# Kernel optimization log

Hardware: AMD Instinct MI355X
Metric: run time of the kernel (lower is better)

## Reference

```python
import jax, jax.numpy as jnp
import numpy as np

B, H, W, C = 4, 64, 64, 256       # C == number_of_filters // 2
NOF = 512
CA = NOF // 8                      # f/g projection dim = 64
CH = NOF // 2                      # h / output projection dim = 256 (== C)


def setup_inputs() -> dict:
    key = jax.random.key(0)
    ks = jax.random.split(key, 10)
    sc = 1.0 / np.sqrt(C)
    x = jax.random.normal(ks[0], (B, H, W, C), jnp.float32)
    Wf = jax.random.normal(ks[1], (C, CA), jnp.float32) * sc
    bf = jnp.zeros((CA,), jnp.float32)
    Wg = jax.random.normal(ks[2], (C, CA), jnp.float32) * sc
    bg = jnp.zeros((CA,), jnp.float32)
    Wh = jax.random.normal(ks[3], (C, CH), jnp.float32) * sc
    bh = jnp.zeros((CH,), jnp.float32)
    Wo = jax.random.normal(ks[4], (CH, CH), jnp.float32) * (1.0 / np.sqrt(CH))
    bo = jnp.zeros((CH,), jnp.float32)
    gamma = jax.random.normal(ks[5], (1,), jnp.float32) * 0.1
    return {"x": x, "Wf": Wf, "bf": bf, "Wg": Wg, "bg": bg,
            "Wh": Wh, "bh": bh, "Wo": Wo, "bo": bo, "gamma": gamma}


def reference(x, Wf, bf, Wg, bg, Wh, bh, Wo, bo, gamma):
    b, h, w, c = x.shape
    n = h * w
    # 1x1 conv projections == per-pixel matmuls over channels
    f = (jnp.einsum('bhwc,cd->bhwd', x, Wf) + bf).reshape(b, n, -1)   # [B,N,CA]
    g = (jnp.einsum('bhwc,cd->bhwd', x, Wg) + bg).reshape(b, n, -1)   # [B,N,CA]
    hh = (jnp.einsum('bhwc,cd->bhwd', x, Wh) + bh).reshape(b, n, -1)  # [B,N,CH]
    # s = g @ f^T : full spatial attention scores [B,N,N]
    s = jnp.einsum('bnd,bmd->bnm', g, f)
    beta = jax.nn.softmax(s, axis=-1)
    o = jnp.einsum('bnm,bmc->bnc', beta, hh).reshape(b, h, w, c)      # CH == C
    # post-attention 1x1 conv
    o2 = jnp.einsum('bhwc,cd->bhwd', o, Wo) + bo
    y = gamma * o2 + x
    return y
```

## Files before the change

kernel.cpp:

```cpp
#include <hip/hip_runtime.h>

typedef __bf16  bf16x8 __attribute__((ext_vector_type(8)));
typedef short   s16x8  __attribute__((ext_vector_type(8)));
typedef float   f32x4  __attribute__((ext_vector_type(4)));
typedef float   f32x16 __attribute__((ext_vector_type(16)));
typedef int     i32x2  __attribute__((ext_vector_type(2)));

#define LOG2E 1.44269504088896f
#define SM_M2 (44.0f * LOG2E)

__device__ __forceinline__ unsigned short f2bf(float f){
  unsigned u = __builtin_bit_cast(unsigned, f);
  return (unsigned short)((u + 0x7fffu + ((u >> 16) & 1u)) >> 16);
}

__device__ __forceinline__ int cvtpk_bf16(float a, float b){
  int r; asm("v_cvt_pk_bf16_f32 %0, %1, %2" : "=v"(r) : "v"(a), "v"(b)); return r;
}

__device__ __forceinline__ float bfhalf2f(unsigned short u){
  unsigned v = ((unsigned)u) << 16; return __builtin_bit_cast(float, v);
}

#define OFF_WTFG 0u
#define OFF_WHT  65536u
#define OFF_WOT  196608u
#define OFF_XBF  327680u
#define OFF_F    8716288u
#define OFF_G    10813440u
#define OFF_HT   12910592u
#define OFF_PART 21299200u
#define OFF_LP   38076416u

__global__ __launch_bounds__(256) void prep(const float* __restrict__ x,
                                            const float* __restrict__ Wf, const float* __restrict__ Wg,
                                            const float* __restrict__ Wh, const float* __restrict__ Wo,
                                            unsigned short* __restrict__ xbf,
                                            unsigned short* __restrict__ WTfg,
                                            unsigned short* __restrict__ WhT,
                                            unsigned short* __restrict__ WoT){
  int bid = blockIdx.x;
  if (bid < 2048) {
    int t = bid * 256 + threadIdx.x;
    const f32x4* xp = (const f32x4*)x;
    f32x4 a = xp[2 * t], b = xp[2 * t + 1];
    s16x8 o;
    o[0] = (short)f2bf(a[0]); o[1] = (short)f2bf(a[1]); o[2] = (short)f2bf(a[2]); o[3] = (short)f2bf(a[3]);
    o[4] = (short)f2bf(b[0]); o[5] = (short)f2bf(b[1]); o[6] = (short)f2bf(b[2]); o[7] = (short)f2bf(b[3]);
    ((s16x8*)xbf)[t] = o;
  } else {
    int t = (bid - 2048) * 256 + threadIdx.x;
    if (t < 32768) {
      int n = t >> 8, k = t & 255;
      float v = (n < 64) ? Wf[k * 64 + n] : Wg[k * 64 + (n - 64)];
      WTfg[t] = f2bf(v);
    } else if (t < 98304) {
      int i = t - 32768; int n = i >> 8, k = i & 255;
      WhT[i] = f2bf(Wh[k * 256 + n]);
    } else {
      int i = t - 98304; int n = i >> 8, k = i & 255;
      WoT[i] = f2bf(Wo[k * 256 + n]);
    }
  }
}

__global__ __launch_bounds__(256) void proj(const unsigned short* __restrict__ xbf,
                                            const unsigned short* __restrict__ WTfg,
                                            const unsigned short* __restrict__ WhT,
                                            const float* __restrict__ bfv, const float* __restrict__ bgv,
                                            const float* __restrict__ bhv,
                                            unsigned short* __restrict__ fK, unsigned short* __restrict__ gQ,
                                            unsigned short* __restrict__ hT){
  int lane = threadIdx.x & 63, widx = threadIdx.x >> 6;
  int l15 = lane & 15, g4 = lane >> 4;
  int bid = blockIdx.x;
  if (bid < 1024) {
    int w = bid * 4 + widx;
    int c0 = (w & 15) * 16;
    int pb = (w >> 4) * 64;
    bf16x8 a[8];
    const unsigned short* wr = WhT + (c0 + l15) * 256 + g4 * 8;
#pragma unroll
    for (int kb = 0; kb < 8; kb++) a[kb] = *(const bf16x8*)(wr + kb * 32);
#pragma unroll
    for (int pt = 0; pt < 4; pt++) {
      int p0 = pb + pt * 16;
      f32x4 acc = {0.f, 0.f, 0.f, 0.f};
      const unsigned short* xr = xbf + (p0 + l15) * 256 + g4 * 8;
#pragma unroll
      for (int kb = 0; kb < 8; kb++) {
        bf16x8 b = *(const bf16x8*)(xr + kb * 32);
        acc = __builtin_amdgcn_mfma_f32_16x16x32_bf16(a[kb], b, acc, 0, 0, 0);
      }
      int bq = p0 >> 12, n0 = p0 & 4095;
      unsigned short* op = hT + bq * (256 * 4096) + n0 + l15;
#pragma unroll
      for (int r = 0; r < 4; r++) {
        int c = c0 + g4 * 4 + r;
        op[c * 4096] = f2bf(acc[r] + bhv[c]);
      }
    }
  } else {
    int w = (bid - 1024) * 4 + widx;
    int p0 = w * 16;
    bf16x8 a[8];
    const unsigned short* xr = xbf + (p0 + l15) * 256 + g4 * 8;
#pragma unroll
    for (int kb = 0; kb < 8; kb++) a[kb] = *(const bf16x8*)(xr + kb * 32);
#pragma unroll
    for (int ct = 0; ct < 8; ct++) {
      int c0 = ct * 16;
      f32x4 acc = {0.f, 0.f, 0.f, 0.f};
      const unsigned short* wr = WTfg + (c0 + l15) * 256 + g4 * 8;
#pragma unroll
      for (int kb = 0; kb < 8; kb++) {
        bf16x8 b = *(const bf16x8*)(wr + kb * 32);
        acc = __builtin_amdgcn_mfma_f32_16x16x32_bf16(a[kb], b, acc, 0, 0, 0);
      }
      float bias = (ct < 4) ? bfv[c0 + l15] : bgv[c0 - 64 + l15];
      unsigned short* outp = (ct < 4) ? (fK + c0 + l15) : (gQ + (c0 - 64) + l15);
#pragma unroll
      for (int r = 0; r < 4; r++) {
        int row = p0 + g4 * 4 + r;
        outp[row * 64] = f2bf(acc[r] + bias);
      }
    }
  }
}

__global__ __launch_bounds__(512, 2) void attn1(const unsigned short* __restrict__ fK,
                                                const unsigned short* __restrict__ gQ,
                                                const unsigned short* __restrict__ hT,
                                                unsigned short* __restrict__ part,
                                                float* __restrict__ lpart){
  __shared__ __attribute__((aligned(16))) char smem[81920];
  const int tid  = threadIdx.x;
  const int lane = tid & 63, w = tid >> 6;
  const int l31  = lane & 31, hi = lane >> 5;
  const int qh   = w >> 1, cs = w & 1;
  const int b    = blockIdx.x & 3;
  const int rest = blockIdx.x >> 2;
  const int qb   = rest >> 1;
  const int kh   = rest & 1;
  const int q0   = qb * 128 + qh * 32;
  const int kbase = kh * 2048;

  const unsigned short* fKb = fK + (size_t)b * 4096 * 64;
  const unsigned short* gQb = gQ + (size_t)b * 4096 * 64;
  const unsigned short* hTb = hT + (size_t)b * 256 * 4096;

  bf16x8 qfr[4];
#pragma unroll
  for (int c4 = 0; c4 < 4; c4++)
    qfr[c4] = *(const bf16x8*)(gQb + (size_t)(q0 + l31) * 64 + c4 * 16 + hi * 8);

  char* buf0 = smem;
  char* buf1 = smem + 32768;
  char* kb0  = smem + 65536;
  char* kb1  = smem + 73728;

  auto STAGE = [&](char* vbuf, char* kbuf, int m0){
    int r = lane >> 3, gl = lane & 7;
#pragma unroll
    for (int k = 0; k < 4; k++){
      int c = 32 * w + k * 8 + r;
      const unsigned short* gp = hTb + (size_t)c * 4096 + m0 + ((gl ^ (c & 7)) * 8);
      __builtin_amdgcn_global_load_lds((const __attribute__((address_space(1))) unsigned int*)gp,
          (__attribute__((address_space(3))) unsigned int*)(vbuf + ((4 * w + k) << 10)), 16, 0, 0);
    }
    {
      int row = 8 * w + r;
      const unsigned short* gp = fKb + (size_t)(m0 + row) * 64 + ((gl ^ r) * 8);
      __builtin_amdgcn_global_load_lds((const __attribute__((address_space(1))) unsigned int*)gp,
          (__attribute__((address_space(3))) unsigned int*)(kbuf + (w << 10)), 16, 0, 0);
    }
  };

  f32x16 acc[4];
#pragma unroll
  for (int ct = 0; ct < 4; ct++)
#pragma unroll
    for (int i = 0; i < 16; i++) acc[ct][i] = 0.f;
  float lvec[16];
#pragma unroll
  for (int i = 0; i < 16; i++) lvec[i] = 0.f;

  auto COMPUTE = [&](const char* kbuf, const char* vbuf){
    bf16x8 Kf[8];
#pragma unroll
    for (int s = 0; s < 2; s++)
#pragma unroll
      for (int c4 = 0; c4 < 4; c4++)
        Kf[s * 4 + c4] = *(const bf16x8*)(kbuf + (s * 32 + l31) * 128 + (((c4 * 2 + hi) ^ (l31 & 7)) << 4));

    f32x16 t0 = {0,0,0,0,0,0,0,0,0,0,0,0,0,0,0,0};
    f32x16 t1 = {0,0,0,0,0,0,0,0,0,0,0,0,0,0,0,0};
#pragma unroll
    for (int c4 = 0; c4 < 4; c4++) t0 = __builtin_amdgcn_mfma_f32_32x32x16_bf16(Kf[c4],     qfr[c4], t0, 0, 0, 0);
#pragma unroll
    for (int c4 = 0; c4 < 4; c4++) t1 = __builtin_amdgcn_mfma_f32_32x32x16_bf16(Kf[4 + c4], qfr[c4], t1, 0, 0, 0);

    float p[32];
#pragma unroll
    for (int r = 0; r < 16; r++) p[r]      = __builtin_amdgcn_exp2f(fmaf(t0[r], LOG2E, -SM_M2));
#pragma unroll
    for (int r = 0; r < 16; r++) p[16 + r] = __builtin_amdgcn_exp2f(fmaf(t1[r], LOG2E, -SM_M2));
#pragma unroll
    for (int r = 0; r < 16; r++) lvec[r] += p[r] + p[16 + r];

    bf16x8 Bf[4];
#pragma unroll
    for (int mc = 0; mc < 4; mc++) {
      int x0 = cvtpk_bf16(p[mc*8+0], p[mc*8+1]);
      int x1 = cvtpk_bf16(p[mc*8+2], p[mc*8+3]);
      int y0 = cvtpk_bf16(p[mc*8+4], p[mc*8+5]);
      int y1 = cvtpk_bf16(p[mc*8+6], p[mc*8+7]);
      int b0, b1, b2, b3;
#if __has_builtin(__builtin_amdgcn_permlane32_swap)
      i32x2 r0 = __builtin_amdgcn_permlane32_swap(x0, y0, false, false);
      i32x2 r1 = __builtin_amdgcn_permlane32_swap(x1, y1, false, false);
      b0 = r0[0]; b1 = r1[0]; b2 = r0[1]; b3 = r1[1];
#else
      int xs0 = __shfl_xor(x0, 32), xs1 = __shfl_xor(x1, 32);
      int ys0 = __shfl_xor(y0, 32), ys1 = __shfl_xor(y1, 32);
      b0 = hi ? ys0 : x0;  b1 = hi ? ys1 : x1;
      b2 = hi ? y0  : xs0; b3 = hi ? y1  : xs1;
#endif
      union { int i[4]; bf16x8 v; } u;
      u.i[0] = b0; u.i[1] = b1; u.i[2] = b2; u.i[3] = b3;
      Bf[mc] = u.v;
    }

#pragma unroll
    for (int mc = 0; mc < 4; mc++) {
#pragma unroll
      for (int ct = 0; ct < 4; ct++) {
        int c = cs * 128 + ct * 32 + l31;
        const char* vp = vbuf + c * 128 + ((((mc * 2 + hi)) ^ (c & 7)) << 4);
        bf16x8 vf = *(const bf16x8*)vp;
        acc[ct] = __builtin_amdgcn_mfma_f32_32x32x16_bf16(vf, Bf[mc], acc[ct], 0, 0, 0);
      }
    }
  };

  STAGE(buf0, kb0, kbase);

  for (int it = 0; it < 32; it += 2) {
    STAGE(buf1, kb1, kbase + (it + 1) * 64);
    asm volatile("s_waitcnt vmcnt(5)" ::: "memory");
    __builtin_amdgcn_sched_barrier(0);
    __builtin_amdgcn_s_barrier();
    __builtin_amdgcn_sched_barrier(0);
    COMPUTE(kb0, buf0);
    __builtin_amdgcn_s_barrier();
    if (it + 2 < 32) {
      STAGE(buf0, kb0, kbase + (it + 2) * 64);
      asm volatile("s_waitcnt vmcnt(5)" ::: "memory");
    } else {
      asm volatile("s_waitcnt vmcnt(0)" ::: "memory");
    }
    __builtin_amdgcn_sched_barrier(0);
    __builtin_amdgcn_s_barrier();
    __builtin_amdgcn_sched_barrier(0);
    COMPUTE(kb1, buf1);
    __builtin_amdgcn_s_barrier();
  }

  float l_part = 0.f;
#pragma unroll
  for (int r = 0; r < 16; r++) l_part += lvec[r];
  l_part += __shfl_xor(l_part, 32);

  size_t tile = (size_t)((b * 32 + qb) * 2 + kh);
  if (cs == 0 && hi == 0)
    lpart[tile * 128 + qh * 32 + l31] = l_part;

  unsigned short* pbase = part + tile * (128 * 256);
  char* obase = smem;
#pragma unroll 1
  for (int ch = 0; ch < 4; ch++) {
    __syncthreads();
    if (qh == ch) {
      int q = l31;
#pragma unroll
      for (int ct = 0; ct < 4; ct++)
#pragma unroll
        for (int r = 0; r < 16; r += 2) {
          int c = cs * 128 + ct * 32 + 8 * (r >> 2) + 4 * hi + (r & 3);
          int u = cvtpk_bf16(acc[ct][r], acc[ct][r + 1]);
          int cb = c * 2;
          *(int*)(obase + q * 512 + (((cb >> 4) ^ (q & 7)) << 4) + (cb & 15)) = u;
        }
    }
    __syncthreads();
    int qq = tid >> 4, i = tid & 15;
#pragma unroll
    for (int j = 0; j < 2; j++) {
      int g = i * 2 + j;
      s16x8 v = *(const s16x8*)(obase + qq * 512 + ((g ^ (qq & 7)) << 4));
      *(s16x8*)(pbase + (ch * 32 + qq) * 256 + g * 8) = v;
    }
  }
}

__global__ __launch_bounds__(512, 2) void merge(const unsigned short* __restrict__ part,
                                                const float* __restrict__ lpart,
                                                const unsigned short* __restrict__ WoT,
                                                const float* __restrict__ bov,
                                                const float* __restrict__ gamma,
                                                const float* __restrict__ x,
                                                float* __restrict__ y){
  __shared__ __attribute__((aligned(16))) char obase[32768];
  const int tid  = threadIdx.x;
  const int lane = tid & 63, w = tid >> 6;
  const int b    = blockIdx.x & 3;
  const int q64  = blockIdx.x >> 2;
  const int qb   = q64 >> 1;
  const int off  = (q64 & 1) * 64;

  size_t t0i = (size_t)((b * 32 + qb) * 2 + 0);
  size_t t1i = (size_t)((b * 32 + qb) * 2 + 1);
  const unsigned short* p0 = part + t0i * (128 * 256) + (size_t)off * 256;
  const unsigned short* p1 = part + t1i * (128 * 256) + (size_t)off * 256;

  {
    int q = tid >> 3, i = tid & 7;
    float inv = 1.0f / (lpart[t0i * 128 + off + q] + lpart[t1i * 128 + off + q]);
#pragma unroll
    for (int j = 0; j < 4; j++) {
      int c0 = i * 32 + j * 8;
      s16x8 v1 = *(const s16x8*)(p0 + q * 256 + c0);
      s16x8 v2 = *(const s16x8*)(p1 + q * 256 + c0);
#pragma unroll
      for (int k = 0; k < 4; k++) {
        float a0 = (bfhalf2f((unsigned short)v1[2*k])   + bfhalf2f((unsigned short)v2[2*k]))   * inv;
        float a1 = (bfhalf2f((unsigned short)v1[2*k+1]) + bfhalf2f((unsigned short)v2[2*k+1])) * inv;
        int c = c0 + 2 * k;
        int u = cvtpk_bf16(a0, a1);
        int cb = c * 2;
        *(int*)(obase + q * 512 + (((cb >> 4) ^ (q & 7)) << 4) + (cb & 15)) = u;
      }
    }
  }
  __syncthreads();
  {
    int l15 = lane & 15, g4 = lane >> 4;
    int q0e = (w & 3) * 16;
    int hf  = w >> 2;
    bf16x8 a[8];
    const char* orl = obase + (size_t)(q0e + l15) * 512;
#pragma unroll
    for (int kb = 0; kb < 8; kb++)
      a[kb] = *(const bf16x8*)(orl + (((kb * 4 + g4) ^ (l15 & 7)) << 4));
    float gm = gamma[0];
#pragma unroll
    for (int ct = 0; ct < 8; ct++) {
      int c0 = hf * 128 + ct * 16;
      f32x4 accp = {0.f, 0.f, 0.f, 0.f};
      const unsigned short* wr = WoT + (c0 + l15) * 256 + g4 * 8;
#pragma unroll
      for (int kb = 0; kb < 8; kb++) {
        bf16x8 bfr = *(const bf16x8*)(wr + kb * 32);
        accp = __builtin_amdgcn_mfma_f32_16x16x32_bf16(a[kb], bfr, accp, 0, 0, 0);
      }
      float bias = bov[c0 + l15];
#pragma unroll
      for (int r = 0; r < 4; r++) {
        int row = (b << 12) + q64 * 64 + q0e + g4 * 4 + r;
        size_t idx = (size_t)row * 256 + c0 + l15;
        y[idx] = gm * (accp[r] + bias) + x[idx];
      }
    }
  }
}

extern "C" void kernel_launch(void* const* d_in, const int* in_sizes, int n_in,
                              void* d_out, int out_size, void* d_ws, size_t ws_size,
                              hipStream_t stream){
  const float* x     = (const float*)d_in[0];
  const float* Wf    = (const float*)d_in[1];
  const float* bfv   = (const float*)d_in[2];
  const float* Wg    = (const float*)d_in[3];
  const float* bgv   = (const float*)d_in[4];
  const float* Wh    = (const float*)d_in[5];
  const float* bhv   = (const float*)d_in[6];
  const float* Wo    = (const float*)d_in[7];
  const float* bov   = (const float*)d_in[8];
  const float* gamma = (const float*)d_in[9];
  float* y = (float*)d_out;

  char* ws = (char*)d_ws;
  unsigned short* WTfg = (unsigned short*)(ws + OFF_WTFG);
  unsigned short* WhT  = (unsigned short*)(ws + OFF_WHT);
  unsigned short* WoT  = (unsigned short*)(ws + OFF_WOT);
  unsigned short* xbf  = (unsigned short*)(ws + OFF_XBF);
  unsigned short* fK   = (unsigned short*)(ws + OFF_F);
  unsigned short* gQ   = (unsigned short*)(ws + OFF_G);
  unsigned short* hT   = (unsigned short*)(ws + OFF_HT);
  unsigned short* part = (unsigned short*)(ws + OFF_PART);
  float*          lp   = (float*)(ws + OFF_LP);

  prep <<<2688, 256, 0, stream>>>(x, Wf, Wg, Wh, Wo, xbf, WTfg, WhT, WoT);
  proj <<<1280, 256, 0, stream>>>(xbf, WTfg, WhT, bfv, bgv, bhv, fK, gQ, hT);
  attn1<<<256, 512, 0, stream>>>(fK, gQ, hT, part, lp);
  merge<<<256, 512, 0, stream>>>(part, lp, WoT, bov, gamma, x, y);
}
```

Before: 124.1 us.

## Stage x tile in LDS for fused f/g/h projection and retile merge

The projection kernel now uses one 768-thread block per 64 pixels. The block loads the x tile once into swizzled LDS with global_load_lds, and all f, g and h output tiles read from that shared copy. This replaces separate blocks that each reread x and the weights from global memory. The merge kernel is retiled into 512 blocks of 256 threads covering 32 query rows each, which halves per-block LDS and spreads the work over more, smaller blocks. In exchange, the grid for projection is smaller, so each wave does more serial work.

```diff
diff --git a/kernel.cpp b/kernel.cpp
--- a/kernel.cpp
+++ b/kernel.cpp
@@ -64,65 +64,82 @@
   }
 }
 
-__global__ __launch_bounds__(256) void proj(const unsigned short* __restrict__ xbf,
+__global__ __launch_bounds__(768) void proj(const unsigned short* __restrict__ xbf,
                                             const unsigned short* __restrict__ WTfg,
                                             const unsigned short* __restrict__ WhT,
                                             const float* __restrict__ bfv, const float* __restrict__ bgv,
                                             const float* __restrict__ bhv,
                                             unsigned short* __restrict__ fK, unsigned short* __restrict__ gQ,
                                             unsigned short* __restrict__ hT){
-  int lane = threadIdx.x & 63, widx = threadIdx.x >> 6;
-  int l15 = lane & 15, g4 = lane >> 4;
-  int bid = blockIdx.x;
-  if (bid < 1024) {
-    int w = bid * 4 + widx;
-    int c0 = (w & 15) * 16;
-    int pb = (w >> 4) * 64;
-    bf16x8 a[8];
-    const unsigned short* wr = WhT + (c0 + l15) * 256 + g4 * 8;
-#pragma unroll
-    for (int kb = 0; kb < 8; kb++) a[kb] = *(const bf16x8*)(wr + kb * 32);
-#pragma unroll
-    for (int pt = 0; pt < 4; pt++) {
-      int p0 = pb + pt * 16;
-      f32x4 acc = {0.f, 0.f, 0.f, 0.f};
-      const unsigned short* xr = xbf + (p0 + l15) * 256 + g4 * 8;
-#pragma unroll
-      for (int kb = 0; kb < 8; kb++) {
-        bf16x8 b = *(const bf16x8*)(xr + kb * 32);
-        acc = __builtin_amdgcn_mfma_f32_16x16x32_bf16(a[kb], b, acc, 0, 0, 0);
-      }
-      int bq = p0 >> 12, n0 = p0 & 4095;
-      unsigned short* op = hT + bq * (256 * 4096) + n0 + l15;
-#pragma unroll
-      for (int r = 0; r < 4; r++) {
-        int c = c0 + g4 * 4 + r;
-        op[c * 4096] = f2bf(acc[r] + bhv[c]);
+  __shared__ __attribute__((aligned(16))) char xt[32768];
+  const int tid = threadIdx.x;
+  const int lane = tid & 63, w = tid >> 6;
+  const int l15 = lane & 15, g4 = lane >> 4;
+  const int p0 = blockIdx.x * 64;
+
+  if (w < 8) {
+    int rp = lane >> 5, gl = lane & 31;
+#pragma unroll
+    for (int k = 0; k < 4; k++) {
+      int row = 8 * w + 2 * k + rp;
+      const unsigned short* gp = xbf + (size_t)(p0 + row) * 256 + ((gl ^ (row & 7)) * 8);
+      __builtin_amdgcn_global_load_lds((const __attribute__((address_space(1))) unsigned int*)gp,
+          (__attribute__((address_space(3))) unsigned int*)(xt + ((4 * w + k) << 10)), 16, 0, 0);
+    }
+  }
+  asm volatile("s_waitcnt vmcnt(0)" ::: "memory");
+  __syncthreads();
+
+  auto XFRAG = [&](int pt, int kb) -> bf16x8 {
+    int row = pt * 16 + l15;
+    return *(const bf16x8*)(xt + row * 512 + (((kb * 4 + g4) ^ (row & 7)) << 4));
+  };
+
+  if (w < 4) {
+#pragma unroll
+    for (int j = 0; j < 2; j++) {
+      int ctg = w * 2 + j, c0 = ctg * 16;
+      bf16x8 bw[8];
+      const unsigned short* wr = WTfg + (c0 + l15) * 256 + g4 * 8;
+#pragma unroll
+      for (int kb = 0; kb < 8; kb++) bw[kb] = *(const bf16x8*)(wr + kb * 32);
+      float bias = (ctg < 4) ? bfv[c0 + l15] : bgv[c0 - 64 + l15];
+      unsigned short* outp = (ctg < 4) ? (fK + c0 + l15) : (gQ + (c0 - 64) + l15);
+#pragma unroll
+      for (int pt = 0; pt < 4; pt++) {
+        f32x4 acc = {0.f, 0.f, 0.f, 0.f};
+#pragma unroll
+        for (int kb = 0; kb < 8; kb++)
+          acc = __builtin_amdgcn_mfma_f32_16x16x32_bf16(XFRAG(pt, kb), bw[kb], acc, 0, 0, 0);
+#pragma unroll
+        for (int r = 0; r < 4; r++) {
+          int row = p0 + pt * 16 + g4 * 4 + r;
+          outp[row * 64] = f2bf(acc[r] + bias);
+        }
       }
     }
   } else {
-    int w = (bid - 1024) * 4 + widx;
-    int p0 = w * 16;
-    bf16x8 a[8];
-    const unsigned short* xr = xbf + (p0 + l15) * 256 + g4 * 8;
-#pragma unroll
-    for (int kb = 0; kb < 8; kb++) a[kb] = *(const bf16x8*)(xr + kb * 32);
-#pragma unroll
-    for (int ct = 0; ct < 8; ct++) {
-      int c0 = ct * 16;
-      f32x4 acc = {0.f, 0.f, 0.f, 0.f};
-      const unsigned short* wr = WTfg + (c0 + l15) * 256 + g4 * 8;
-#pragma unroll
-      for (int kb = 0; kb < 8; kb++) {
-        bf16x8 b = *(const bf16x8*)(wr + kb * 32);
-        acc = __builtin_amdgcn_mfma_f32_16x16x32_bf16(a[kb], b, acc, 0, 0, 0);
-      }
-      float bias = (ct < 4) ? bfv[c0 + l15] : bgv[c0 - 64 + l15];
-      unsigned short* outp = (ct < 4) ? (fK + c0 + l15) : (gQ + (c0 - 64) + l15);
-#pragma unroll
-      for (int r = 0; r < 4; r++) {
-        int row = p0 + g4 * 4 + r;
-        outp[row * 64] = f2bf(acc[r] + bias);
+#pragma unroll
+    for (int j = 0; j < 2; j++) {
+      int c0 = ((w - 4) * 2 + j) * 16;
+      bf16x8 a[8];
+      const unsigned short* wr = WhT + (c0 + l15) * 256 + g4 * 8;
+#pragma unroll
+      for (int kb = 0; kb < 8; kb++) a[kb] = *(const bf16x8*)(wr + kb * 32);
+#pragma unroll
+      for (int pt = 0; pt < 4; pt++) {
+        f32x4 acc = {0.f, 0.f, 0.f, 0.f};
+#pragma unroll
+        for (int kb = 0; kb < 8; kb++)
+          acc = __builtin_amdgcn_mfma_f32_16x16x32_bf16(a[kb], XFRAG(pt, kb), acc, 0, 0, 0);
+        int pg = p0 + pt * 16;
+        int bq = pg >> 12, n0 = pg & 4095;
+        unsigned short* op = hT + bq * (256 * 4096) + n0 + l15;
+#pragma unroll
+        for (int r = 0; r < 4; r++) {
+          int c = c0 + g4 * 4 + r;
+          op[c * 4096] = f2bf(acc[r] + bhv[c]);
+        }
       }
     }
   }
@@ -303,23 +320,23 @@
   }
 }
 
-__global__ __launch_bounds__(512, 2) void merge(const unsigned short* __restrict__ part,
+__global__ __launch_bounds__(256, 2) void merge(const unsigned short* __restrict__ part,
                                                 const float* __restrict__ lpart,
                                                 const unsigned short* __restrict__ WoT,
                                                 const float* __restrict__ bov,
                                                 const float* __restrict__ gamma,
                                                 const float* __restrict__ x,
                                                 float* __restrict__ y){
-  __shared__ __attribute__((aligned(16))) char obase[32768];
+  __shared__ __attribute__((aligned(16))) char obase[16384];
   const int tid  = threadIdx.x;
   const int lane = tid & 63, w = tid >> 6;
   const int b    = blockIdx.x & 3;
-  const int q64  = blockIdx.x >> 2;
-  const int qb   = q64 >> 1;
-  const int off  = (q64 & 1) * 64;
+  const int rest = blockIdx.x >> 2;
+  const int qb   = rest >> 2;
+  const int off  = (rest & 3) * 32;
 
   size_t t0i = (size_t)((b * 32 + qb) * 2 + 0);
-  size_t t1i = (size_t)((b * 32 + qb) * 2 + 1);
+  size_t t1i = t0i + 1;
   const unsigned short* p0 = part + t0i * (128 * 256) + (size_t)off * 256;
   const unsigned short* p1 = part + t1i * (128 * 256) + (size_t)off * 256;
 
@@ -345,8 +362,8 @@
   __syncthreads();
   {
     int l15 = lane & 15, g4 = lane >> 4;
-    int q0e = (w & 3) * 16;
-    int hf  = w >> 2;
+    int q0e = (w & 1) * 16;
+    int hf  = w >> 1;
     bf16x8 a[8];
     const char* orl = obase + (size_t)(q0e + l15) * 512;
 #pragma unroll
@@ -366,7 +383,7 @@
       float bias = bov[c0 + l15];
 #pragma unroll
       for (int r = 0; r < 4; r++) {
-        int row = (b << 12) + q64 * 64 + q0e + g4 * 4 + r;
+        int row = (b << 12) + qb * 128 + off + q0e + g4 * 4 + r;
         size_t idx = (size_t)row * 256 + c0 + l15;
         y[idx] = gm * (accp[r] + bias) + x[idx];
       }
@@ -401,7 +418,7 @@
   float*          lp   = (float*)(ws + OFF_LP);
 
   prep <<<2688, 256, 0, stream>>>(x, Wf, Wg, Wh, Wo, xbf, WTfg, WhT, WoT);
-  proj <<<1280, 256, 0, stream>>>(xbf, WTfg, WhT, bfv, bgv, bhv, fK, gQ, hT);
+  proj <<<256, 768, 0, stream>>>(xbf, WTfg, WhT, bfv, bgv, bhv, fK, gQ, hT);
   attn1<<<256, 512, 0, stream>>>(fK, gQ, hT, part, lp);
-  merge<<<256, 512, 0, stream>>>(part, lp, WoT, bov, gamma, x, y);
-}
+  merge<<<512, 256, 0, stream>>>(part, lp, WoT, bov, gamma, x, y);
+}
```

Result: faster. 104.9 us (-15.5%).
